# Optimization experiments

Measured on AMD Instinct MI355X. Metric: run time of the kernel, lower is better.

Reference implementation:

```python
import jax, jax.numpy as jnp
import numpy as np

B, V, CIN, H, W = 2, 4, 256, 96, 96
COUT, VS = 32, 64


def setup_inputs() -> dict:
    key = jax.random.key(0)
    k1, k2, k3, k4, k5 = jax.random.split(key, 5)
    features = jax.random.normal(k1, (B, V, CIN, H, W), dtype=jnp.float32)
    proj_matricies = jax.random.normal(k2, (B, V, 3, 4), dtype=jnp.float32)
    coord_volumes = jax.random.normal(k3, (B, VS, VS, VS, 3), dtype=jnp.float32) * 1000.0
    W_proc = jax.random.normal(k4, (COUT, CIN), dtype=jnp.float32) * 0.05
    b_proc = jax.random.normal(k5, (COUT,), dtype=jnp.float32) * 0.01
    return {"features": features, "proj_matricies": proj_matricies,
            "coord_volumes": coord_volumes, "W_proc": W_proc, "b_proc": b_proc}


def _bilinear_sample(feat, x, y):
    # feat: [C, H, W]; x, y: [N] pixel coords (align_corners=True mapping already applied)
    Hh, Ww = feat.shape[1], feat.shape[2]
    x0 = jnp.floor(x).astype(jnp.int32); x1 = x0 + 1
    y0 = jnp.floor(y).astype(jnp.int32); y1 = y0 + 1
    wx1 = x - x0; wx0 = 1.0 - wx1
    wy1 = y - y0; wy0 = 1.0 - wy1

    def gather(xi, yi):
        valid = ((xi >= 0) & (xi < Ww) & (yi >= 0) & (yi < Hh)).astype(feat.dtype)
        xc = jnp.clip(xi, 0, Ww - 1); yc = jnp.clip(yi, 0, Hh - 1)
        return feat[:, yc, xc] * valid  # [C, N] (zeros padding)

    return (gather(x0, y0) * (wx0 * wy0)
            + gather(x1, y0) * (wx1 * wy0)
            + gather(x0, y1) * (wx0 * wy1)
            + gather(x1, y1) * (wx1 * wy1))


def reference(features, proj_matricies, coord_volumes, W_proc, b_proc):
    b, v, cin, h, w = features.shape
    vs = coord_volumes.shape[1]
    # 1x1 conv (process_feature)
    feats = jnp.einsum('bvchw,oc->bvohw', features, W_proc) + b_proc[None, None, :, None, None]
    c = feats.shape[2]
    # homogeneous 3D grid points: [B, N, 4]
    pts = coord_volumes.reshape(b, -1, 3)
    pts_h = jnp.concatenate([pts, jnp.ones(pts.shape[:-1] + (1,), pts.dtype)], axis=-1)
    # project to image plane: [B, V, N, 3] homogeneous (u, v, w)
    proj_pts = jnp.einsum('bvij,bnj->bvni', proj_matricies, pts_h)
    wz = proj_pts[..., 2]
    invalid = wz <= 0.0
    wz_safe = jnp.where(wz == 0.0, 1.0, wz)
    u = proj_pts[..., 0] / wz_safe
    ve = proj_pts[..., 1] / wz_safe
    # normalized grid coords (faithful to original: x divided by feature_shape[0]=H, y by feature_shape[1]=W)
    gx = 2.0 * (u / h - 0.5)
    gy = 2.0 * (ve / w - 0.5)
    # align_corners=True pixel coords: x indexes width, y indexes height
    px = (gx + 1.0) * 0.5 * (w - 1)
    py = (gy + 1.0) * 0.5 * (h - 1)
    # sample per (batch, view): [B, V, C, N]
    sampled = jax.vmap(jax.vmap(_bilinear_sample))(feats, px, py)
    sampled = jnp.where(invalid[:, :, None, :], 0.0, sampled)
    # softmax over views per (b, c, voxel), weighted sum
    weights = jax.nn.softmax(sampled, axis=1)
    vol = jnp.sum(sampled * weights, axis=1)  # [B, C, N]
    return vol.reshape(b, c, vs, vs, vs)
```

## Files before the change

kernel.cpp:

```cpp
#include <hip/hip_runtime.h>
#include <hip/hip_bf16.h>

#define CIN   256
#define COUT  32
#define IMG_H 96
#define IMG_W 96
#define HW    (IMG_H*IMG_W)
#define NB    2
#define NV    4
#define VSZ   64
#define NVOX  (VSZ*VSZ*VSZ)

typedef __attribute__((ext_vector_type(2))) float f32x2;

__device__ __forceinline__ float fast_exp2(float x) {
    float r;
    asm("v_exp_f32 %0, %1" : "=v"(r) : "v"(x));
    return r;
}

__global__ __launch_bounds__(256) void conv1x1_kernel(
    const float* __restrict__ features,
    const float* __restrict__ Wp,
    const float* __restrict__ bp,
    __hip_bfloat16* __restrict__ out)
{
    const int og   = __builtin_amdgcn_readfirstlane((threadIdx.x >> 6) & 3);
    const int lane = threadIdx.x & 63;
    const int bv   = blockIdx.y;
    const int px   = blockIdx.x*64 + lane;
    const float* f     = features + (size_t)bv*CIN*HW + px;
    const float* wbase = Wp + (size_t)og*8*CIN;

    float acc[8];
    #pragma unroll
    for (int j = 0; j < 8; ++j) acc[j] = bp[og*8 + j];

    for (int cc = 0; cc < CIN; cc += 8) {
        float x[8];
        #pragma unroll
        for (int i = 0; i < 8; ++i)
            x[i] = f[(size_t)(cc + i)*HW];
        #pragma unroll
        for (int i = 0; i < 8; ++i) {
            #pragma unroll
            for (int j = 0; j < 8; ++j)
                acc[j] += x[i] * wbase[(size_t)j*CIN + cc + i];
        }
    }

    union { uint4 u4; __hip_bfloat16 h[8]; } pk;
    #pragma unroll
    for (int j = 0; j < 8; ++j) pk.h[j] = __float2bfloat16(acc[j]);
    *(uint4*)(out + ((size_t)(bv*HW + px))*COUT + og*8) = pk.u4;
}

__global__ __launch_bounds__(256, 4) void volgen_kernel(
    const __hip_bfloat16* __restrict__ feats,
    const float* __restrict__ proj,
    const float* __restrict__ coords,
    float* __restrict__ out)
{
    const int tid = threadIdx.x;
    const int b   = blockIdx.y;
    const int n   = blockIdx.x*256 + tid;

    const float* cp = coords + ((size_t)b*NVOX + n)*3;
    const float X = cp[0], Y = cp[1], Z = cp[2];

    const float LOG2E = 1.4426950408889634f;

    int   off[NV][4];
    float wgt[NV][4];
    #pragma unroll
    for (int v = 0; v < NV; ++v) {
        const float* P = proj + (size_t)(b*NV + v)*12;
        const float wz = P[8]*X + P[9]*Y + P[10]*Z + P[11];
        const bool  vz = wz > 0.f;
        const float rz = __builtin_amdgcn_rcpf(wz);
        float px = (P[0]*X + P[1]*Y + P[2]*Z + P[3]) * rz * (95.f/96.f);
        float py = (P[4]*X + P[5]*Y + P[6]*Z + P[7]) * rz * (95.f/96.f);
        px = vz ? px : 0.f;  py = vz ? py : 0.f;
        px = fminf(fmaxf(px, -1.0e6f), 1.0e6f);
        py = fminf(fmaxf(py, -1.0e6f), 1.0e6f);
        const float fx0 = floorf(px), fy0 = floorf(py);
        const int x0 = (int)fx0, y0 = (int)fy0, x1 = x0+1, y1 = y0+1;
        const float wx1 = px - fx0, wx0 = 1.f - wx1;
        const float wy1 = py - fy0, wy0 = 1.f - wy1;
        const bool vx0 = (unsigned)x0 < (unsigned)IMG_W;
        const bool vx1 = (unsigned)x1 < (unsigned)IMG_W;
        const bool vy0 = (unsigned)y0 < (unsigned)IMG_H;
        const bool vy1 = (unsigned)y1 < (unsigned)IMG_H;
        const int cx0 = min(max(x0, 0), IMG_W-1), cx1 = min(max(x1, 0), IMG_W-1);
        const int cy0 = min(max(y0, 0), IMG_H-1), cy1 = min(max(y1, 0), IMG_H-1);
        const int base = ((b*NV + v)*HW)*COUT*2;
        off[v][0] = base + (cy0*IMG_W + cx0)*(COUT*2);  wgt[v][0] = (vz & vx0 & vy0) ? wx0*wy0*LOG2E : 0.f;
        off[v][1] = base + (cy0*IMG_W + cx1)*(COUT*2);  wgt[v][1] = (vz & vx1 & vy0) ? wx1*wy0*LOG2E : 0.f;
        off[v][2] = base + (cy1*IMG_W + cx0)*(COUT*2);  wgt[v][2] = (vz & vx0 & vy1) ? wx0*wy1*LOG2E : 0.f;
        off[v][3] = base + (cy1*IMG_W + cx1)*(COUT*2);  wgt[v][3] = (vz & vx1 & vy1) ? wx1*wy1*LOG2E : 0.f;
    }

    const char* fb = (const char*)feats;
    const size_t ob = (size_t)b*COUT*NVOX + n;
    const float LN2 = 0.6931471805599453f;

    for (int ch0 = 0; ch0 < COUT; ch0 += 8) {
        f32x2 A2[4], B2[4];
        uint4 t[4], tn[4];

        #pragma unroll
        for (int c = 0; c < 4; ++c)
            t[c] = *(const uint4*)(fb + off[0][c] + ch0*2);

        #pragma unroll
        for (int v = 0; v < NV; ++v) {
            if (v < NV-1) {
                #pragma unroll
                for (int c = 0; c < 4; ++c)
                    tn[c] = *(const uint4*)(fb + off[v+1][c] + ch0*2);
            }

            f32x2 s2[4];
            #pragma unroll
            for (int c = 0; c < 4; ++c) {
                const float w = wgt[v][c];
                const f32x2 w2 = { w, w };
                const unsigned tu[4] = { t[c].x, t[c].y, t[c].z, t[c].w };
                #pragma unroll
                for (int k = 0; k < 4; ++k) {
                    f32x2 f2;
                    f2.x = __uint_as_float(tu[k] << 16);
                    f2.y = __uint_as_float(tu[k] & 0xffff0000u);
                    if (c == 0) s2[k] = w2 * f2;
                    else        s2[k] += w2 * f2;
                }
            }

            #pragma unroll
            for (int k = 0; k < 4; ++k) {
                f32x2 e2;
                e2.x = fast_exp2(s2[k].x);
                e2.y = fast_exp2(s2[k].y);
                if (v == 0) { A2[k] = e2;  B2[k] = s2[k]*e2; }
                else        { A2[k] += e2; B2[k] += s2[k]*e2; }
            }

            if (v < NV-1) {
                #pragma unroll
                for (int c = 0; c < 4; ++c) t[c] = tn[c];
            }
        }

        #pragma unroll
        for (int k = 0; k < 4; ++k) {
            out[ob + (size_t)(ch0 + 2*k    )*NVOX] = B2[k].x * __builtin_amdgcn_rcpf(A2[k].x) * LN2;
            out[ob + (size_t)(ch0 + 2*k + 1)*NVOX] = B2[k].y * __builtin_amdgcn_rcpf(A2[k].y) * LN2;
        }
    }
}

extern "C" void kernel_launch(void* const* d_in, const int* in_sizes, int n_in,
                              void* d_out, int out_size, void* d_ws, size_t ws_size,
                              hipStream_t stream)
{
    const float* features = (const float*)d_in[0];
    const float* proj     = (const float*)d_in[1];
    const float* coords   = (const float*)d_in[2];
    const float* Wp       = (const float*)d_in[3];
    const float* bp       = (const float*)d_in[4];
    float* out = (float*)d_out;
    __hip_bfloat16* featsT = (__hip_bfloat16*)d_ws;

    hipLaunchKernelGGL(conv1x1_kernel, dim3(HW/64, NB*NV), dim3(256), 0, stream,
                       features, Wp, bp, featsT);
    hipLaunchKernelGGL(volgen_kernel, dim3(NVOX/256, NB), dim3(256), 0, stream,
                       featsT, proj, coords, out);
}
```

Baseline: 179.0 us.

## Split conv1x1 input channels across waves and reduce partial sums in LDS

The 1x1 conv kernel now uses 512-thread blocks covering 128 pixels. Each wave computes 16 output channels over half of the input channels. Partial sums are combined through shared memory and the bias is added before the bf16 store. This reads each feature element half as many times across output-channel groups and raises per-thread ILP, at the cost of LDS traffic, a barrier, and more registers.

```diff
diff --git a/kernel.cpp b/kernel.cpp
--- a/kernel.cpp
+++ b/kernel.cpp
@@ -19,24 +19,29 @@
     return r;
 }
 
-__global__ __launch_bounds__(256) void conv1x1_kernel(
+__global__ __launch_bounds__(512) void conv1x1_kernel(
     const float* __restrict__ features,
     const float* __restrict__ Wp,
     const float* __restrict__ bp,
     __hip_bfloat16* __restrict__ out)
 {
-    const int og   = __builtin_amdgcn_readfirstlane((threadIdx.x >> 6) & 3);
+    __shared__ float red[2][COUT][128];
+    const int wid  = threadIdx.x >> 6;
+    const int pxs  = __builtin_amdgcn_readfirstlane(wid & 1);
+    const int og   = __builtin_amdgcn_readfirstlane((wid >> 1) & 1);
+    const int kh   = __builtin_amdgcn_readfirstlane(wid >> 2);
     const int lane = threadIdx.x & 63;
+    const int pxl  = pxs*64 + lane;
     const int bv   = blockIdx.y;
-    const int px   = blockIdx.x*64 + lane;
-    const float* f     = features + (size_t)bv*CIN*HW + px;
-    const float* wbase = Wp + (size_t)og*8*CIN;
+    const int px   = blockIdx.x*128 + pxl;
+    const float* f     = features + (size_t)bv*CIN*HW + (size_t)kh*128*HW + px;
+    const float* wbase = Wp + (size_t)og*16*CIN + kh*128;
 
-    float acc[8];
+    float acc[16];
     #pragma unroll
-    for (int j = 0; j < 8; ++j) acc[j] = bp[og*8 + j];
+    for (int j = 0; j < 16; ++j) acc[j] = 0.f;
 
-    for (int cc = 0; cc < CIN; cc += 8) {
+    for (int cc = 0; cc < 128; cc += 8) {
         float x[8];
         #pragma unroll
         for (int i = 0; i < 8; ++i)
@@ -44,15 +49,27 @@
         #pragma unroll
         for (int i = 0; i < 8; ++i) {
             #pragma unroll
-            for (int j = 0; j < 8; ++j)
+            for (int j = 0; j < 16; ++j)
                 acc[j] += x[i] * wbase[(size_t)j*CIN + cc + i];
         }
     }
 
-    union { uint4 u4; __hip_bfloat16 h[8]; } pk;
     #pragma unroll
-    for (int j = 0; j < 8; ++j) pk.h[j] = __float2bfloat16(acc[j]);
-    *(uint4*)(out + ((size_t)(bv*HW + px))*COUT + og*8) = pk.u4;
+    for (int j = 0; j < 16; ++j)
+        red[kh][og*16 + j][pxl] = acc[j];
+    __syncthreads();
+
+    if (kh == 0) {
+        union { uint4 u4[2]; __hip_bfloat16 hh[16]; } pk;
+        #pragma unroll
+        for (int j = 0; j < 16; ++j) {
+            const int ch = og*16 + j;
+            pk.hh[j] = __float2bfloat16(red[0][ch][pxl] + red[1][ch][pxl] + bp[ch]);
+        }
+        __hip_bfloat16* op = out + (size_t)(bv*HW + px)*COUT + og*16;
+        *(uint4*)(op)     = pk.u4[0];
+        *(uint4*)(op + 8) = pk.u4[1];
+    }
 }
 
 __global__ __launch_bounds__(256, 4) void volgen_kernel(
@@ -171,7 +188,7 @@
     float* out = (float*)d_out;
     __hip_bfloat16* featsT = (__hip_bfloat16*)d_ws;
 
-    hipLaunchKernelGGL(conv1x1_kernel, dim3(HW/64, NB*NV), dim3(256), 0, stream,
+    hipLaunchKernelGGL(conv1x1_kernel, dim3(HW/128, NB*NV), dim3(512), 0, stream,
                        features, Wp, bp, featsT);
     hipLaunchKernelGGL(volgen_kernel, dim3(NVOX/256, NB), dim3(256), 0, stream,
                        featsT, proj, coords, out);
```

Result: no change. 179.8 us (+0.4%).

## Split views across four lanes per voxel and reduce softmax with shuffles

Applied to the files above, without the earlier changes.

The volume kernel now gives each view to its own lane, so four lanes share one voxel, and the grid grows fourfold. Each lane projects and gathers only its view's four corners. The softmax numerator and denominator are summed across the lane quad with xor shuffles, and each lane writes two of the eight channels. The goal is lower register pressure, higher occupancy and more independent gathers in flight, at the cost of shuffle instructions, redundant coordinate loads and output stores that are strided across lanes and less coalesced.

```diff
diff --git a/kernel.cpp b/kernel.cpp
--- a/kernel.cpp
+++ b/kernel.cpp
@@ -63,98 +63,107 @@
 {
     const int tid = threadIdx.x;
     const int b   = blockIdx.y;
-    const int n   = blockIdx.x*256 + tid;
+    const int vq  = tid & 3;
+    const int n   = blockIdx.x*64 + (tid >> 2);
 
     const float* cp = coords + ((size_t)b*NVOX + n)*3;
     const float X = cp[0], Y = cp[1], Z = cp[2];
 
     const float LOG2E = 1.4426950408889634f;
 
-    int   off[NV][4];
-    float wgt[NV][4];
-    #pragma unroll
-    for (int v = 0; v < NV; ++v) {
-        const float* P = proj + (size_t)(b*NV + v)*12;
-        const float wz = P[8]*X + P[9]*Y + P[10]*Z + P[11];
-        const bool  vz = wz > 0.f;
-        const float rz = __builtin_amdgcn_rcpf(wz);
-        float px = (P[0]*X + P[1]*Y + P[2]*Z + P[3]) * rz * (95.f/96.f);
-        float py = (P[4]*X + P[5]*Y + P[6]*Z + P[7]) * rz * (95.f/96.f);
-        px = vz ? px : 0.f;  py = vz ? py : 0.f;
-        px = fminf(fmaxf(px, -1.0e6f), 1.0e6f);
-        py = fminf(fmaxf(py, -1.0e6f), 1.0e6f);
-        const float fx0 = floorf(px), fy0 = floorf(py);
-        const int x0 = (int)fx0, y0 = (int)fy0, x1 = x0+1, y1 = y0+1;
-        const float wx1 = px - fx0, wx0 = 1.f - wx1;
-        const float wy1 = py - fy0, wy0 = 1.f - wy1;
-        const bool vx0 = (unsigned)x0 < (unsigned)IMG_W;
-        const bool vx1 = (unsigned)x1 < (unsigned)IMG_W;
-        const bool vy0 = (unsigned)y0 < (unsigned)IMG_H;
-        const bool vy1 = (unsigned)y1 < (unsigned)IMG_H;
-        const int cx0 = min(max(x0, 0), IMG_W-1), cx1 = min(max(x1, 0), IMG_W-1);
-        const int cy0 = min(max(y0, 0), IMG_H-1), cy1 = min(max(y1, 0), IMG_H-1);
-        const int base = ((b*NV + v)*HW)*COUT*2;
-        off[v][0] = base + (cy0*IMG_W + cx0)*(COUT*2);  wgt[v][0] = (vz & vx0 & vy0) ? wx0*wy0*LOG2E : 0.f;
-        off[v][1] = base + (cy0*IMG_W + cx1)*(COUT*2);  wgt[v][1] = (vz & vx1 & vy0) ? wx1*wy0*LOG2E : 0.f;
-        off[v][2] = base + (cy1*IMG_W + cx0)*(COUT*2);  wgt[v][2] = (vz & vx0 & vy1) ? wx0*wy1*LOG2E : 0.f;
-        off[v][3] = base + (cy1*IMG_W + cx1)*(COUT*2);  wgt[v][3] = (vz & vx1 & vy1) ? wx1*wy1*LOG2E : 0.f;
-    }
+    const float* P = proj + (size_t)(b*NV + vq)*12;
+    const float wz = P[8]*X + P[9]*Y + P[10]*Z + P[11];
+    const bool  vz = wz > 0.f;
+    const float rz = __builtin_amdgcn_rcpf(wz);
+    float px = (P[0]*X + P[1]*Y + P[2]*Z + P[3]) * rz * (95.f/96.f);
+    float py = (P[4]*X + P[5]*Y + P[6]*Z + P[7]) * rz * (95.f/96.f);
+    px = vz ? px : 0.f;  py = vz ? py : 0.f;
+    px = fminf(fmaxf(px, -1.0e6f), 1.0e6f);
+    py = fminf(fmaxf(py, -1.0e6f), 1.0e6f);
+    const float fx0 = floorf(px), fy0 = floorf(py);
+    const int x0 = (int)fx0, y0 = (int)fy0, x1 = x0+1, y1 = y0+1;
+    const float wx1 = px - fx0, wx0 = 1.f - wx1;
+    const float wy1 = py - fy0, wy0 = 1.f - wy1;
+    const bool vx0 = (unsigned)x0 < (unsigned)IMG_W;
+    const bool vx1 = (unsigned)x1 < (unsigned)IMG_W;
+    const bool vy0 = (unsigned)y0 < (unsigned)IMG_H;
+    const bool vy1 = (unsigned)y1 < (unsigned)IMG_H;
+    const int cx0 = min(max(x0, 0), IMG_W-1), cx1 = min(max(x1, 0), IMG_W-1);
+    const int cy0 = min(max(y0, 0), IMG_H-1), cy1 = min(max(y1, 0), IMG_H-1);
+    const int base = ((b*NV + vq)*HW)*COUT*2;
+    int   off[4];
+    float wgt[4];
+    off[0] = base + (cy0*IMG_W + cx0)*(COUT*2);  wgt[0] = (vz & vx0 & vy0) ? wx0*wy0*LOG2E : 0.f;
+    off[1] = base + (cy0*IMG_W + cx1)*(COUT*2);  wgt[1] = (vz & vx1 & vy0) ? wx1*wy0*LOG2E : 0.f;
+    off[2] = base + (cy1*IMG_W + cx0)*(COUT*2);  wgt[2] = (vz & vx0 & vy1) ? wx0*wy1*LOG2E : 0.f;
+    off[3] = base + (cy1*IMG_W + cx1)*(COUT*2);  wgt[3] = (vz & vx1 & vy1) ? wx1*wy1*LOG2E : 0.f;
 
     const char* fb = (const char*)feats;
     const size_t ob = (size_t)b*COUT*NVOX + n;
     const float LN2 = 0.6931471805599453f;
 
+    uint4 t[4], tn[4];
+    #pragma unroll
+    for (int c = 0; c < 4; ++c)
+        t[c] = *(const uint4*)(fb + off[c]);
+
+    #pragma unroll
     for (int ch0 = 0; ch0 < COUT; ch0 += 8) {
-        f32x2 A2[4], B2[4];
-        uint4 t[4], tn[4];
+        if (ch0 + 8 < COUT) {
+            #pragma unroll
+            for (int c = 0; c < 4; ++c)
+                tn[c] = *(const uint4*)(fb + off[c] + (ch0 + 8)*2);
+        }
 
+        f32x2 s2[4];
         #pragma unroll
-        for (int c = 0; c < 4; ++c)
-            t[c] = *(const uint4*)(fb + off[0][c] + ch0*2);
-
-        #pragma unroll
-        for (int v = 0; v < NV; ++v) {
-            if (v < NV-1) {
-                #pragma unroll
-                for (int c = 0; c < 4; ++c)
-                    tn[c] = *(const uint4*)(fb + off[v+1][c] + ch0*2);
-            }
-
-            f32x2 s2[4];
-            #pragma unroll
-            for (int c = 0; c < 4; ++c) {
-                const float w = wgt[v][c];
-                const f32x2 w2 = { w, w };
-                const unsigned tu[4] = { t[c].x, t[c].y, t[c].z, t[c].w };
-                #pragma unroll
-                for (int k = 0; k < 4; ++k) {
-                    f32x2 f2;
-                    f2.x = __uint_as_float(tu[k] << 16);
-                    f2.y = __uint_as_float(tu[k] & 0xffff0000u);
-                    if (c == 0) s2[k] = w2 * f2;
-                    else        s2[k] += w2 * f2;
-                }
-            }
-
+        for (int c = 0; c < 4; ++c) {
+            const float w = wgt[c];
+            const f32x2 w2 = { w, w };
+            const unsigned tu[4] = { t[c].x, t[c].y, t[c].z, t[c].w };
             #pragma unroll
             for (int k = 0; k < 4; ++k) {
-                f32x2 e2;
-                e2.x = fast_exp2(s2[k].x);
-                e2.y = fast_exp2(s2[k].y);
-                if (v == 0) { A2[k] = e2;  B2[k] = s2[k]*e2; }
-                else        { A2[k] += e2; B2[k] += s2[k]*e2; }
-            }
-
-            if (v < NV-1) {
-                #pragma unroll
-                for (int c = 0; c < 4; ++c) t[c] = tn[c];
+                f32x2 f2;
+                f2.x = __uint_as_float(tu[k] << 16);
+                f2.y = __uint_as_float(tu[k] & 0xffff0000u);
+                if (c == 0) s2[k] = w2 * f2;
+                else        s2[k] += w2 * f2;
             }
         }
 
+        f32x2 A2[4], B2[4];
         #pragma unroll
         for (int k = 0; k < 4; ++k) {
-            out[ob + (size_t)(ch0 + 2*k    )*NVOX] = B2[k].x * __builtin_amdgcn_rcpf(A2[k].x) * LN2;
-            out[ob + (size_t)(ch0 + 2*k + 1)*NVOX] = B2[k].y * __builtin_amdgcn_rcpf(A2[k].y) * LN2;
+            f32x2 e2;
+            e2.x = fast_exp2(s2[k].x);
+            e2.y = fast_exp2(s2[k].y);
+            A2[k] = e2;
+            B2[k] = s2[k]*e2;
+        }
+
+        #pragma unroll
+        for (int m = 1; m <= 2; m <<= 1) {
+            #pragma unroll
+            for (int k = 0; k < 4; ++k) {
+                A2[k].x += __shfl_xor(A2[k].x, m, 64);
+                A2[k].y += __shfl_xor(A2[k].y, m, 64);
+                B2[k].x += __shfl_xor(B2[k].x, m, 64);
+                B2[k].y += __shfl_xor(B2[k].y, m, 64);
+            }
+        }
+
+        const f32x2 Alo = (vq & 1) ? A2[1] : A2[0];
+        const f32x2 Ahi = (vq & 1) ? A2[3] : A2[2];
+        const f32x2 Aq  = (vq & 2) ? Ahi : Alo;
+        const f32x2 Blo = (vq & 1) ? B2[1] : B2[0];
+        const f32x2 Bhi = (vq & 1) ? B2[3] : B2[2];
+        const f32x2 Bq  = (vq & 2) ? Bhi : Blo;
+        out[ob + (size_t)(ch0 + 2*vq    )*NVOX] = Bq.x * __builtin_amdgcn_rcpf(Aq.x) * LN2;
+        out[ob + (size_t)(ch0 + 2*vq + 1)*NVOX] = Bq.y * __builtin_amdgcn_rcpf(Aq.y) * LN2;
+
+        if (ch0 + 8 < COUT) {
+            #pragma unroll
+            for (int c = 0; c < 4; ++c) t[c] = tn[c];
         }
     }
 }
@@ -173,6 +182,6 @@
 
     hipLaunchKernelGGL(conv1x1_kernel, dim3(HW/64, NB*NV), dim3(256), 0, stream,
                        features, Wp, bp, featsT);
-    hipLaunchKernelGGL(volgen_kernel, dim3(NVOX/256, NB), dim3(256), 0, stream,
+    hipLaunchKernelGGL(volgen_kernel, dim3(NVOX/64, NB), dim3(256), 0, stream,
                        featsT, proj, coords, out);
 }
```

Result: slower. 208.9 us (+16.7%).
